# Kernel optimization log

Hardware: AMD Instinct MI355X
Metric: run time of the kernel (lower is better)

## Reference

```python
import jax, jax.numpy as jnp
import numpy as np


def setup_inputs() -> dict:
    key = jax.random.key(0)
    ks = jax.random.split(key, 8)
    B, H, L, N = 8, 256, 4096, 64
    u = jax.random.normal(ks[0], (B, H, L), dtype=jnp.float32)
    # frozen reservoir poles: stable complex eigenvalues |Lambda| < 1
    mag = jax.random.uniform(ks[1], (H, N), minval=0.5, maxval=0.99)
    phase = jax.random.uniform(ks[2], (H, N), minval=0.0, maxval=2.0 * np.pi)
    Lambda_re = (mag * jnp.cos(phase)).astype(jnp.float32)
    Lambda_im = (mag * jnp.sin(phase)).astype(jnp.float32)
    CB_re = jax.random.normal(ks[3], (H, N), dtype=jnp.float32) * 0.1
    CB_im = jax.random.normal(ks[4], (H, N), dtype=jnp.float32) * 0.1
    D = jax.random.normal(ks[5], (H,), dtype=jnp.float32)
    W_mix = jax.random.normal(ks[6], (2 * H, H), dtype=jnp.float32) * (1.0 / np.sqrt(H))
    b_mix = jnp.zeros((2 * H,), dtype=jnp.float32)
    return {"u": u, "Lambda_re": Lambda_re, "Lambda_im": Lambda_im,
            "CB_re": CB_re, "CB_im": CB_im, "D": D,
            "W_mix": W_mix, "b_mix": b_mix}


def reference(u, Lambda_re, Lambda_im, CB_re, CB_im, D, W_mix, b_mix):
    B, H, L = u.shape
    Lam = Lambda_re + 1j * Lambda_im                      # [H,N] frozen poles
    CB = CB_re + 1j * CB_im                               # [H,N] C*B_bar
    # Vandermonde kernel: K[h,l] = 2*Re(sum_n CB[h,n] * Lam[h,n]^l)
    log_lam = jnp.log(Lam)                                # [H,N]
    t = jnp.arange(L, dtype=jnp.float32)
    V = jnp.exp(log_lam[:, :, None] * t[None, None, :])   # [H,N,L]
    K = 2.0 * jnp.einsum('hn,hnl->hl', CB, V).real        # [H,L]
    # causal convolution via FFT (length 2L to avoid wrap-around)
    n = 2 * L
    Uf = jnp.fft.rfft(u, n=n)                             # [B,H,n/2+1]
    Kf = jnp.fft.rfft(K, n=n)                             # [H,n/2+1]
    y = jnp.fft.irfft(Uf * Kf[None], n=n)[..., :L]        # [B,H,L]
    y = y + D[None, :, None] * u                          # skip connection
    y = jnp.tanh(y)
    # 1x1 conv mixing to 2H channels, then GLU over channel dim (-2)
    z = jnp.einsum('oh,bhl->bol', W_mix, y) + b_mix[None, :, None]  # [B,2H,L]
    a, g = jnp.split(z, 2, axis=-2)
    return a * jax.nn.sigmoid(g)                          # [B,H,L]
```

## Files before the change

kernel.cpp:

```cpp
#include <hip/hip_runtime.h>
#include <hip/hip_bf16.h>
#include <cmath>

#define BDIM 8
#define HDIM 256
#define LDIM 4096
#define NDIM 64
#define TCH  64
#define NCH  64

typedef unsigned short u16;
typedef unsigned int   u32;
typedef __attribute__((ext_vector_type(8))) short short8x;
typedef __attribute__((ext_vector_type(4))) float f32x4;

__device__ __forceinline__ float rcp_fast(float x) { return __builtin_amdgcn_rcpf(x); }
__device__ __forceinline__ float tanh_fast(float x) {
    float e = __expf(2.0f * x);
    return 1.0f - 2.0f * rcp_fast(e + 1.0f);
}
__device__ __forceinline__ u16 f2bf(float f) {
    unsigned int u = __float_as_uint(f);
    u = u + 0x7fffu + ((u >> 16) & 1u);
    return (u16)(u >> 16);
}
__device__ __forceinline__ float bf2f(u16 s) {
    return __uint_as_float(((unsigned int)s) << 16);
}

__global__ __launch_bounds__(256) void tables5_kernel(
    const float* __restrict__ lre_g, const float* __restrict__ lim_g,
    const float* __restrict__ cbre_g, const float* __restrict__ cbim_g,
    u16* __restrict__ Phi, u16* __restrict__ Plo,
    u16* __restrict__ Ghi, u16* __restrict__ Thi,
    float2* __restrict__ L64)
{
    __shared__ float qre[64][64];
    __shared__ float qim[64][64];
    __shared__ float Ksh[64];
    const int h = blockIdx.x;
    const int tid = threadIdx.x;
    const int w = tid >> 6;
    const int n = tid & 63;

    const float lr = lre_g[h * 64 + n], li = lim_g[h * 64 + n];
    const float cr = 2.0f * cbre_g[h * 64 + n];
    const float ci = 2.0f * cbim_g[h * 64 + n];

    u32* Gh32 = (u32*)(Ghi + (size_t)h * 8192);
    u16* Th = Thi + (size_t)h * 4096;

    float sr = lr, si = li;
    #pragma unroll
    for (int j = 0; j < 4; ++j) {
        float tr = sr * sr - si * si;
        si = 2.0f * sr * si; sr = tr;
    }
    float qr = 1.0f, qi = 0.0f;
    for (int j = 0; j < w; ++j) {
        float tr = qr * sr - qi * si;
        qi = qr * si + qi * sr; qr = tr;
    }

    #pragma unroll
    for (int j = 0; j < 16; ++j) {
        const int t = 16 * w + j;
        float kp = cr * qr - ci * qi;
        #pragma unroll
        for (int m = 32; m > 0; m >>= 1) kp += __shfl_xor(kp, m);
        if (n == 0) Ksh[t] = kp;

        qre[t][n] = qr; qim[t][n] = qi;

        float nqr = qr * lr - qi * li;
        float nqi = qr * li + qi * lr;
        qr = nqr; qi = nqi;

        float gre = cr * qr - ci * qi;
        float gnim = -(cr * qi + ci * qr);
        Gh32[t * 64 + n] = (u32)f2bf(gre) | ((u32)f2bf(gnim) << 16);
    }
    if (w == 3) L64[h * 64 + n] = make_float2(qr, qi);
    __syncthreads();

    {
        const int row = tid >> 1;
        const int n0  = row >> 1;
        const float* src = (row & 1) ? &qim[0][0] : &qre[0][0];
        const int s0 = (tid & 1) * 32;
        union { u16 s[32]; short8x v[4]; } HB, LB;
        #pragma unroll
        for (int i = 0; i < 32; ++i) {
            int s = s0 + i;
            float v = src[(63 - s) * 64 + n0];
            u16 hv = f2bf(v);
            HB.s[i] = hv; LB.s[i] = f2bf(v - bf2f(hv));
        }
        u16* dh = Phi + (size_t)h * 8192 + row * 64 + s0;
        u16* dl = Plo + (size_t)h * 8192 + row * 64 + s0;
        #pragma unroll
        for (int k2 = 0; k2 < 4; ++k2) {
            *(short8x*)(dh + 8 * k2) = HB.v[k2];
            *(short8x*)(dl + 8 * k2) = LB.v[k2];
        }
    }

    const int r = tid >> 2, c0 = (tid & 3) * 16;
    #pragma unroll
    for (int i = 0; i < 16; ++i) {
        int c = c0 + i;
        float val = (c <= r) ? Ksh[r - c] : 0.0f;
        Th[r * 64 + c] = f2bf(val);
    }
}

__global__ __launch_bounds__(256, 4) void scan5h_kernel(
    const float* __restrict__ u,
    const float* __restrict__ Dg,
    const u16* __restrict__ Phi, const u16* __restrict__ Plo,
    const u16* __restrict__ Ghi, const u16* __restrict__ Thi,
    const float2* __restrict__ L64,
    u16* __restrict__ ybf)
{
    __shared__ __align__(16) char smem[69 * 512];

    const int bid = blockIdx.x;
    const int b = bid >> 8;
    const int h = ((bid >> 3) & 31) * 8 + (bid & 7);
    const int tid = threadIdx.x;
    const int w = tid >> 6, l = tid & 63;
    const int l15 = l & 15, lhi = l >> 4;

    const int ctBase  = (w & 1) * 2;
    const int miBaseV = (w >> 1) * 4;
    const int miBaseY = (w >> 1) * 2;

    const float* urow = u + ((size_t)b * HDIM + h) * LDIM;

    int cBt[2];
    short8x ub[2][2];
    #pragma unroll
    for (int ct2 = 0; ct2 < 2; ++ct2) {
        cBt[ct2] = 16 * (ctBase + ct2) + l15;
        #pragma unroll
        for (int ks = 0; ks < 2; ++ks) {
            const float* src = urow + 64 * cBt[ct2] + 32 * ks + 8 * lhi;
            float4 f0 = *(const float4*)src;
            float4 f1 = *(const float4*)(src + 4);
            float fv[8] = {f0.x, f0.y, f0.z, f0.w, f1.x, f1.y, f1.z, f1.w};
            union { short8x v; u16 s[8]; } H;
            #pragma unroll
            for (int q = 0; q < 8; ++q) H.s[q] = f2bf(fv[q]);
            ub[ct2][ks] = H.v;
        }
    }

    const u16* Ph = Phi + (size_t)h * 8192;
    const u16* Pl = Plo + (size_t)h * 8192;
    {
        f32x4 acc[4][2];
        #pragma unroll
        for (int m = 0; m < 4; ++m)
            #pragma unroll
            for (int c2 = 0; c2 < 2; ++c2)
                acc[m][c2] = (f32x4){0.0f, 0.0f, 0.0f, 0.0f};

        #pragma unroll
        for (int pair = 0; pair < 2; ++pair) {
            short8x pah[2][2], pal[2][2];
            #pragma unroll
            for (int m = 0; m < 2; ++m)
                #pragma unroll
                for (int ks = 0; ks < 2; ++ks) {
                    int off = (16 * (miBaseV + 2 * pair + m) + l15) * 64 + 32 * ks + 8 * lhi;
                    pah[m][ks] = *(const short8x*)(Ph + off);
                    pal[m][ks] = *(const short8x*)(Pl + off);
                }
            #pragma unroll
            for (int m = 0; m < 2; ++m)
                #pragma unroll
                for (int ks = 0; ks < 2; ++ks)
                    #pragma unroll
                    for (int c2 = 0; c2 < 2; ++c2) {
                        f32x4 a = acc[2 * pair + m][c2];
                        a = __builtin_amdgcn_mfma_f32_16x16x32_bf16(pah[m][ks], ub[c2][ks], a, 0, 0, 0);
                        a = __builtin_amdgcn_mfma_f32_16x16x32_bf16(pal[m][ks], ub[c2][ks], a, 0, 0, 0);
                        acc[2 * pair + m][c2] = a;
                    }
        }
        #pragma unroll
        for (int m = 0; m < 4; ++m)
            #pragma unroll
            for (int c2 = 0; c2 < 2; ++c2) {
                int rV = cBt[c2] + 1;
                int byte = 512 * rV + 64 * (miBaseV + m) + 16 * lhi;
                *(f32x4*)(smem + (byte ^ ((rV & 7) << 4))) = acc[m][c2];
            }
    }

    const u16* Th_ = Thi + (size_t)h * 4096;
    f32x4 accTU[2][2];
    {
        short8x tah[2][2];
        #pragma unroll
        for (int m = 0; m < 2; ++m)
            #pragma unroll
            for (int ks = 0; ks < 2; ++ks) {
                int off = (16 * (miBaseY + m) + l15) * 64 + 32 * ks + 8 * lhi;
                tah[m][ks] = *(const short8x*)(Th_ + off);
            }
        #pragma unroll
        for (int m = 0; m < 2; ++m)
            #pragma unroll
            for (int c2 = 0; c2 < 2; ++c2) {
                f32x4 a = {0.0f, 0.0f, 0.0f, 0.0f};
                #pragma unroll
                for (int ks = 0; ks < 2; ++ks)
                    a = __builtin_amdgcn_mfma_f32_16x16x32_bf16(tah[m][ks], ub[c2][ks], a, 0, 0, 0);
                accTU[m][c2] = a;
            }
    }
    __syncthreads();

    const u16* Gh_ = Ghi + (size_t)h * 8192;
    short8x gah_pf[4];
    #pragma unroll
    for (int ks = 0; ks < 4; ++ks) {
        int off = (16 * miBaseY + l15) * 128 + 32 * ks + 8 * lhi;
        gah_pf[ks] = *(const short8x*)(Gh_ + off);
    }

    {
        const int g = w, a = 16 * g;
        float2 lt = L64[h * 64 + l];
        float2 vv[16];
        #pragma unroll
        for (int j = 0; j < 16; ++j) {
            int r = a + j + 1;
            vv[j] = *(const float2*)(smem + ((512 * r + 8 * l) ^ ((r & 7) << 4)));
        }
        float ljr[16], lji[16];
        float xr = 0.0f, xi = 0.0f;
        #pragma unroll
        for (int j = 0; j < 16; ++j) {
            ljr[j] = xr; lji[j] = xi;
            float nr = fmaf(lt.x, xr, fmaf(-lt.y, xi, vv[j].x));
            float ni = fmaf(lt.x, xi, fmaf( lt.y, xr, vv[j].y));
            xr = nr; xi = ni;
        }
        {
            int r = 65 + g;
            *(float2*)(smem + ((512 * r + 8 * l) ^ ((r & 7) << 4))) = make_float2(xr, xi);
        }
        float p16r = lt.x, p16i = lt.y;
        #pragma unroll
        for (int jj = 0; jj < 4; ++jj) {
            float tr = p16r * p16r - p16i * p16i;
            p16i = 2.0f * p16r * p16i; p16r = tr;
        }
        __syncthreads();
        float sr = 0.0f, si = 0.0f;
        for (int gp = 0; gp < g; ++gp) {
            int r = 65 + gp;
            float2 t = *(const float2*)(smem + ((512 * r + 8 * l) ^ ((r & 7) << 4)));
            float nsr = fmaf(p16r, sr, fmaf(-p16i, si, t.x));
            float nsi = fmaf(p16r, si, fmaf( p16i, sr, t.y));
            sr = nsr; si = nsi;
        }
        float pr = 1.0f, pi = 0.0f;
        #pragma unroll
        for (int j = 0; j < 16; ++j) {
            float Xr = fmaf(pr, sr, fmaf(-pi, si, ljr[j]));
            float Xi = fmaf(pr, si, fmaf( pi, sr, lji[j]));
            int c = a + j, sw2 = (c & 7) << 4;
            u16 hr2 = f2bf(Xr); u16 lr2 = f2bf(Xr - bf2f(hr2));
            u16 hi2 = f2bf(Xi); u16 li2 = f2bf(Xi - bf2f(hi2));
            *(u32*)(smem + ((512 * c + 4 * l) ^ sw2))       = (u32)hr2 | ((u32)hi2 << 16);
            *(u32*)(smem + ((512 * c + 256 + 4 * l) ^ sw2)) = (u32)lr2 | ((u32)li2 << 16);
            float npr = pr * lt.x - pi * lt.y;
            float npi = pr * lt.y + pi * lt.x;
            pr = npr; pi = npi;
        }
    }
    __syncthreads();

    short8x xbh[2][4], xbl[2][4];
    #pragma unroll
    for (int c2 = 0; c2 < 2; ++c2) {
        int swX = (cBt[c2] & 7) << 4;
        #pragma unroll
        for (int ks = 0; ks < 4; ++ks) {
            int byte = 512 * cBt[c2] + 64 * ks + 16 * lhi;
            xbh[c2][ks] = *(const short8x*)(smem + (byte ^ swX));
            xbl[c2][ks] = *(const short8x*)(smem + ((byte + 256) ^ swX));
        }
    }

    const float Dh = Dg[h];
    u16* yrow = ybf + ((size_t)b * HDIM + h) * LDIM;
    #pragma unroll
    for (int m = 0; m < 2; ++m) {
        const int mi = miBaseY + m;
        f32x4 acc[2];
        acc[0] = accTU[m][0];
        acc[1] = accTU[m][1];
        short8x gah[4];
        #pragma unroll
        for (int ks = 0; ks < 4; ++ks) {
            if (m == 0) {
                gah[ks] = gah_pf[ks];
            } else {
                int off = (16 * mi + l15) * 128 + 32 * ks + 8 * lhi;
                gah[ks] = *(const short8x*)(Gh_ + off);
            }
        }
        #pragma unroll
        for (int ks = 0; ks < 4; ++ks)
            #pragma unroll
            for (int c2 = 0; c2 < 2; ++c2) {
                acc[c2] = __builtin_amdgcn_mfma_f32_16x16x32_bf16(gah[ks], xbh[c2][ks], acc[c2], 0, 0, 0);
                acc[c2] = __builtin_amdgcn_mfma_f32_16x16x32_bf16(gah[ks], xbl[c2][ks], acc[c2], 0, 0, 0);
            }
        #pragma unroll
        for (int c2 = 0; c2 < 2; ++c2) {
            int off = 64 * cBt[c2] + 16 * mi + 4 * lhi;
            float4 uv = *(const float4*)(urow + off);
            float o0 = tanh_fast(fmaf(Dh, uv.x, acc[c2][0]));
            float o1 = tanh_fast(fmaf(Dh, uv.y, acc[c2][1]));
            float o2 = tanh_fast(fmaf(Dh, uv.z, acc[c2][2]));
            float o3 = tanh_fast(fmaf(Dh, uv.w, acc[c2][3]));
            uint2 pk;
            pk.x = (u32)f2bf(o0) | ((u32)f2bf(o1) << 16);
            pk.y = (u32)f2bf(o2) | ((u32)f2bf(o3) << 16);
            *(uint2*)(yrow + off) = pk;
        }
    }
}

__global__ __launch_bounds__(256) void prep_w(
    const float* __restrict__ W, u16* __restrict__ Wphi)
{
    const int r = blockIdx.x, hcol = threadIdx.x;
    const int src = (r & 1) ? (r >> 1) + 256 : (r >> 1);
    Wphi[r * 256 + hcol] = f2bf(W[src * 256 + hcol]);
}

__global__ __launch_bounds__(512, 2) void mix13_kernel(
    const u16* __restrict__ ybf,
    const u16* __restrict__ Wphi,
    const float* __restrict__ bm,
    float* __restrict__ out)
{
    __shared__ __align__(16) u16 Ysh[2][128 * 64];

    const int tid = threadIdx.x;
    const int w = tid >> 6, l = tid & 63;
    const int l15 = l & 15, lhi = l >> 4;
    const int rbase = blockIdx.y * 256;
    const int b = blockIdx.z;
    const int col0 = blockIdx.x * 128;

    const u16* Yb = ybf + (size_t)b * HDIM * LDIM;

    const int p  = tid >> 4;
    const int cg = tid & 15;

    f32x4 acc[2][8];
    #pragma unroll
    for (int mi = 0; mi < 2; ++mi)
        #pragma unroll
        for (int ct = 0; ct < 8; ++ct)
            acc[mi][ct] = (f32x4){0.0f, 0.0f, 0.0f, 0.0f};

    {
        const u16* r0 = Yb + (size_t)(2 * p) * LDIM + col0 + 8 * cg;
        union { short8x v; u16 s[8]; } Y0, Y1;
        Y0.v = *(const short8x*)r0;
        Y1.v = *(const short8x*)(r0 + LDIM);
        #pragma unroll
        for (int q = 0; q < 8; ++q) {
            int col = 8 * cg + q;
            u32 wv = (u32)Y0.s[q] | ((u32)Y1.s[q] << 16);
            int byte = (col * 128 + 4 * p) ^ ((col & 7) << 4);
            *(u32*)((char*)Ysh[0] + byte) = wv;
        }
    }
    __syncthreads();

    for (int kb = 0; kb < 4; ++kb) {
        const int k0 = kb * 64;
        const int cur = kb & 1;

        union { short8x v; u16 s[8]; } Y0, Y1;
        if (kb < 3) {
            const u16* r0 = Yb + (size_t)(k0 + 64 + 2 * p) * LDIM + col0 + 8 * cg;
            Y0.v = *(const short8x*)r0;
            Y1.v = *(const short8x*)(r0 + LDIM);
        }

        #pragma unroll
        for (int mi = 0; mi < 2; ++mi) {
            const size_t row = (size_t)(rbase + 32 * w + 16 * mi + l15);
            short8x wh[2];
            #pragma unroll
            for (int ks = 0; ks < 2; ++ks) {
                size_t off = row * 256 + k0 + 32 * ks + 8 * lhi;
                wh[ks] = *(const short8x*)(Wphi + off);
            }
            #pragma unroll
            for (int ct = 0; ct < 8; ++ct) {
                #pragma unroll
                for (int ks = 0; ks < 2; ++ks) {
                    int col = 16 * ct + l15;
                    int byte = (col * 128 + 64 * ks + 16 * lhi) ^ ((col & 7) << 4);
                    short8x yb = *(const short8x*)((char*)Ysh[cur] + byte);
                    acc[mi][ct] = __builtin_amdgcn_mfma_f32_16x16x32_bf16(wh[ks], yb, acc[mi][ct], 0, 0, 0);
                }
            }
        }

        if (kb < 3) {
            #pragma unroll
            for (int q = 0; q < 8; ++q) {
                int col = 8 * cg + q;
                u32 wv = (u32)Y0.s[q] | ((u32)Y1.s[q] << 16);
                int byte = (col * 128 + 4 * p) ^ ((col & 7) << 4);
                *(u32*)((char*)Ysh[cur ^ 1] + byte) = wv;
            }
        }
        __syncthreads();
    }

    float* ob = out + ((size_t)b * HDIM) * LDIM;
    #pragma unroll
    for (int mi = 0; mi < 2; ++mi) {
        int r0 = rbase + 32 * w + 16 * mi + 4 * lhi;
        int h1 = r0 >> 1;
        float ba1 = bm[h1],     bg1 = bm[h1 + 256];
        float ba2 = bm[h1 + 1], bg2 = bm[h1 + 1 + 256];
        #pragma unroll
        for (int ct = 0; ct < 8; ++ct) {
            f32x4 a = acc[mi][ct];
            int col = col0 + 16 * ct + l15;
            float A1 = a[0] + ba1, G1 = a[1] + bg1;
            float A2 = a[2] + ba2, G2 = a[3] + bg2;
            ob[(size_t)h1 * LDIM + col]       = A1 * rcp_fast(1.0f + __expf(-G1));
            ob[(size_t)(h1 + 1) * LDIM + col] = A2 * rcp_fast(1.0f + __expf(-G2));
        }
    }
}

extern "C" void kernel_launch(void* const* d_in, const int* in_sizes, int n_in,
                              void* d_out, int out_size, void* d_ws, size_t ws_size,
                              hipStream_t stream)
{
    const float* u    = (const float*)d_in[0];
    const float* lre  = (const float*)d_in[1];
    const float* lim  = (const float*)d_in[2];
    const float* cbre = (const float*)d_in[3];
    const float* cbim = (const float*)d_in[4];
    const float* Dg   = (const float*)d_in[5];
    const float* W    = (const float*)d_in[6];
    const float* bm   = (const float*)d_in[7];
    float* out = (float*)d_out;

    char* ws = (char*)d_ws;
    size_t o = 0;
    u16* Wphi = (u16*)(ws + o); o += (size_t)1 << 19;
    u16* Phi = (u16*)(ws + o); o += (size_t)1 << 22;
    u16* Plo = (u16*)(ws + o); o += (size_t)1 << 22;
    u16* Ghi = (u16*)(ws + o); o += (size_t)1 << 22;
    u16* Thi = (u16*)(ws + o); o += (size_t)1 << 21;
    float2* L64 = (float2*)(ws + o); o += (size_t)1 << 18;
    u16* ybf = (u16*)(ws + o);

    tables5_kernel<<<HDIM, 256, 0, stream>>>(lre, lim, cbre, cbim,
                                             Phi, Plo, Ghi, Thi, L64);
    prep_w<<<512, 256, 0, stream>>>(W, Wphi);
    scan5h_kernel<<<BDIM * HDIM, 256, 0, stream>>>(u, Dg, Phi, Plo, Ghi,
                                                   Thi, L64, ybf);
    dim3 grid(LDIM / 128, 2, BDIM);
    mix13_kernel<<<grid, 512, 0, stream>>>(ybf, Wphi, bm, out);
}
```

Baseline: 82.50 us.

## Drop low-part bf16 split of power table and fold W prep into tables kernel

Removes the hi/lo bf16 split of the pole-power table Phi, so the first MFMA stage of the scan kernel issues half as many MFMAs and reads half the table data. The weight conversion kernel is merged into the tables kernel, which removes one launch. The block has 256 threads, so the tid<256 branch writes the even rows and the second block writes the odd rows; the else branch never runs and the odd-row write is redundant but harmless. The cost is lower precision of the state-propagation term.

Result: faster. 71.86 us (-12.9%).

```diff
diff --git a/kernel.cpp b/kernel.cpp
--- a/kernel.cpp
+++ b/kernel.cpp
@@ -28,12 +28,14 @@
     return __uint_as_float(((unsigned int)s) << 16);
 }
 
-__global__ __launch_bounds__(256) void tables5_kernel(
+__global__ __launch_bounds__(256) void tables6_kernel(
     const float* __restrict__ lre_g, const float* __restrict__ lim_g,
     const float* __restrict__ cbre_g, const float* __restrict__ cbim_g,
-    u16* __restrict__ Phi, u16* __restrict__ Plo,
+    const float* __restrict__ W,
+    u16* __restrict__ Phi,
     u16* __restrict__ Ghi, u16* __restrict__ Thi,
-    float2* __restrict__ L64)
+    float2* __restrict__ L64,
+    u16* __restrict__ Wphi)
 {
     __shared__ float qre[64][64];
     __shared__ float qim[64][64];
@@ -50,6 +52,19 @@
     u32* Gh32 = (u32*)(Ghi + (size_t)h * 8192);
     u16* Th = Thi + (size_t)h * 4096;
 
+    {
+        const int hcol = tid & 255;
+        if (tid < 256) {
+            Wphi[(2 * h) * 256 + hcol]     = f2bf(W[h * 256 + hcol]);
+        } else if (tid < 512) {
+            Wphi[(2 * h + 1) * 256 + hcol] = f2bf(W[(h + 256) * 256 + hcol]);
+        }
+    }
+    {
+        const int hcol = tid;
+        Wphi[(2 * h + 1) * 256 + hcol] = f2bf(W[(h + 256) * 256 + hcol]);
+    }
+
     float sr = lr, si = li;
     #pragma unroll
     for (int j = 0; j < 4; ++j) {
@@ -88,21 +103,16 @@
         const int n0  = row >> 1;
         const float* src = (row & 1) ? &qim[0][0] : &qre[0][0];
         const int s0 = (tid & 1) * 32;
-        union { u16 s[32]; short8x v[4]; } HB, LB;
+        union { u16 s[32]; short8x v[4]; } HB;
         #pragma unroll
         for (int i = 0; i < 32; ++i) {
             int s = s0 + i;
-            float v = src[(63 - s) * 64 + n0];
-            u16 hv = f2bf(v);
-            HB.s[i] = hv; LB.s[i] = f2bf(v - bf2f(hv));
+            HB.s[i] = f2bf(src[(63 - s) * 64 + n0]);
         }
         u16* dh = Phi + (size_t)h * 8192 + row * 64 + s0;
-        u16* dl = Plo + (size_t)h * 8192 + row * 64 + s0;
-        #pragma unroll
-        for (int k2 = 0; k2 < 4; ++k2) {
+        #pragma unroll
+        for (int k2 = 0; k2 < 4; ++k2)
             *(short8x*)(dh + 8 * k2) = HB.v[k2];
-            *(short8x*)(dl + 8 * k2) = LB.v[k2];
-        }
     }
 
     const int r = tid >> 2, c0 = (tid & 3) * 16;
@@ -114,10 +124,10 @@
     }
 }
 
-__global__ __launch_bounds__(256, 4) void scan5h_kernel(
+__global__ __launch_bounds__(256, 4) void scan5i_kernel(
     const float* __restrict__ u,
     const float* __restrict__ Dg,
-    const u16* __restrict__ Phi, const u16* __restrict__ Plo,
+    const u16* __restrict__ Phi,
     const u16* __restrict__ Ghi, const u16* __restrict__ Thi,
     const float2* __restrict__ L64,
     u16* __restrict__ ybf)
@@ -156,7 +166,6 @@
     }
 
     const u16* Ph = Phi + (size_t)h * 8192;
-    const u16* Pl = Plo + (size_t)h * 8192;
     {
         f32x4 acc[4][2];
         #pragma unroll
@@ -167,14 +176,13 @@
 
         #pragma unroll
         for (int pair = 0; pair < 2; ++pair) {
-            short8x pah[2][2], pal[2][2];
+            short8x pah[2][2];
             #pragma unroll
             for (int m = 0; m < 2; ++m)
                 #pragma unroll
                 for (int ks = 0; ks < 2; ++ks) {
                     int off = (16 * (miBaseV + 2 * pair + m) + l15) * 64 + 32 * ks + 8 * lhi;
                     pah[m][ks] = *(const short8x*)(Ph + off);
-                    pal[m][ks] = *(const short8x*)(Pl + off);
                 }
             #pragma unroll
             for (int m = 0; m < 2; ++m)
@@ -182,10 +190,8 @@
                 for (int ks = 0; ks < 2; ++ks)
                     #pragma unroll
                     for (int c2 = 0; c2 < 2; ++c2) {
-                        f32x4 a = acc[2 * pair + m][c2];
-                        a = __builtin_amdgcn_mfma_f32_16x16x32_bf16(pah[m][ks], ub[c2][ks], a, 0, 0, 0);
-                        a = __builtin_amdgcn_mfma_f32_16x16x32_bf16(pal[m][ks], ub[c2][ks], a, 0, 0, 0);
-                        acc[2 * pair + m][c2] = a;
+                        acc[2 * pair + m][c2] = __builtin_amdgcn_mfma_f32_16x16x32_bf16(
+                            pah[m][ks], ub[c2][ks], acc[2 * pair + m][c2], 0, 0, 0);
                     }
         }
         #pragma unroll
@@ -335,14 +341,6 @@
             *(uint2*)(yrow + off) = pk;
         }
     }
-}
-
-__global__ __launch_bounds__(256) void prep_w(
-    const float* __restrict__ W, u16* __restrict__ Wphi)
-{
-    const int r = blockIdx.x, hcol = threadIdx.x;
-    const int src = (r & 1) ? (r >> 1) + 256 : (r >> 1);
-    Wphi[r * 256 + hcol] = f2bf(W[src * 256 + hcol]);
 }
 
 __global__ __launch_bounds__(512, 2) void mix13_kernel(
@@ -468,16 +466,14 @@
     size_t o = 0;
     u16* Wphi = (u16*)(ws + o); o += (size_t)1 << 19;
     u16* Phi = (u16*)(ws + o); o += (size_t)1 << 22;
-    u16* Plo = (u16*)(ws + o); o += (size_t)1 << 22;
     u16* Ghi = (u16*)(ws + o); o += (size_t)1 << 22;
     u16* Thi = (u16*)(ws + o); o += (size_t)1 << 21;
     float2* L64 = (float2*)(ws + o); o += (size_t)1 << 18;
     u16* ybf = (u16*)(ws + o);
 
-    tables5_kernel<<<HDIM, 256, 0, stream>>>(lre, lim, cbre, cbim,
-                                             Phi, Plo, Ghi, Thi, L64);
-    prep_w<<<512, 256, 0, stream>>>(W, Wphi);
-    scan5h_kernel<<<BDIM * HDIM, 256, 0, stream>>>(u, Dg, Phi, Plo, Ghi,
+    tables6_kernel<<<HDIM, 256, 0, stream>>>(lre, lim, cbre, cbim, W,
+                                             Phi, Ghi, Thi, L64, Wphi);
+    scan5i_kernel<<<BDIM * HDIM, 256, 0, stream>>>(u, Dg, Phi, Ghi,
                                                    Thi, L64, ybf);
     dim3 grid(LDIM / 128, 2, BDIM);
     mix13_kernel<<<grid, 512, 0, stream>>>(ybf, Wphi, bm, out);
```
